# Optimization experiments

Measured on AMD Instinct MI355X. Metric: run time of the kernel, lower is better.

Reference implementation:

```python
import jax, jax.numpy as jnp
import numpy as np

N_MOL, N_ATOM, DEG = 32, 128, 32
N = N_MOL * N_ATOM          # 4096 real atoms (no blanks)
P = N * DEG                 # 131072 pairs
N_SENS = 20
SOFT_MIN, SOFT_MAX, HARD_MAX = 0.7, 5.0, 7.5
N_IN, N_OUT, N_HIST = 2, 3, 3
NF1 = 20                    # hipnn1 n_features
NF0 = 2 * NF1               # hipnn0 n_features (doubled in __init__)
NG = 4 * NF1                # gate logits width of InteractLayer W
N_ATOM_LAYERS = 3
NIN0 = 2 + N_HIST           # one-hot over {1,8} + x_h channels


def setup_inputs():
    rng = np.random.default_rng(0)
    species = 1 + 7 * rng.integers(0, 2, size=(N_MOL, N_ATOM))  # values in {1,8}, all nonblank
    base = np.repeat(np.arange(N), DEG)
    local = base % N_ATOM
    neigh = (local + 1 + rng.integers(0, N_ATOM - 1, size=P)) % N_ATOM  # neighbor != self
    pair_second = (base // N_ATOM) * N_ATOM + neigh                     # same-molecule pairs
    key = jax.random.key(0)
    ks = jax.random.split(key, 20)
    g = lambda i, shape, s=0.1: jax.random.normal(ks[i], shape, dtype=jnp.float32) * s
    return {
        "species": jnp.asarray(species, jnp.int32),
        "coordinates": jax.random.uniform(ks[0], (N_MOL, N_ATOM, 3), jnp.float32, 0.0, 6.0),
        "x_h": g(1, (N_MOL, N_ATOM, N_HIST)),
        "x_raw": g(2, (N_MOL, N_ATOM, N_IN)),
        "pair_first": jnp.asarray(base, jnp.int32),
        "pair_second": jnp.asarray(pair_second, jnp.int32),
        "h0_int_w": g(3, (N_SENS, NIN0, NF0)),
        "h0_self_w": g(4, (NIN0, NF0)),
        "h0_self_b": g(5, (NF0,)),
        "h0_aw": g(6, (N_ATOM_LAYERS, NF0, NF0)),
        "h0_ab": g(7, (N_ATOM_LAYERS, NF0)),
        "h1_int_w": g(8, (N_SENS, 1, NF1)),
        "h1_self_w": g(9, (1, NF1)),
        "h1_self_b": g(10, (NF1,)),
        "h1_aw": g(11, (N_ATOM_LAYERS, NF1, NF1)),
        "h1_ab": g(12, (N_ATOM_LAYERS, NF1)),
        "W_int_w": g(13, (N_SENS, NF0, NG)),
        "W_self_w": g(14, (NF0, NG)),
        "W_self_b": g(15, (NG,)),
        "pw0": g(16, (NIN0, 1)),
        "pw1": g(17, (NF1, 1)),
        "pb1": g(18, (1,)),
    }


def _sensitivity(d):
    # inverse-distance gaussian sensitivities with smooth hard cutoff
    mu = jnp.linspace(1.0 / SOFT_MAX, 1.0 / SOFT_MIN, N_SENS)
    sigma = (1.0 / SOFT_MIN - 1.0 / SOFT_MAX) / N_SENS
    sense = jnp.exp(-0.5 * jnp.square((1.0 / d[:, None] - mu) / sigma))
    cut = jnp.where(d < HARD_MAX, jnp.square(jnp.cos(jnp.pi * d / (2.0 * HARD_MAX))), 0.0)
    return sense * cut[:, None]                                     # (P, n_sens)


def _interact(x, sense, pf, ps, int_w, self_w, self_b):
    # gather neighbor features, weight by sensitivities, scatter-add to center atom
    msg = sense[:, :, None] * x[ps][:, None, :]                     # (P, ns, fin)
    env = jax.ops.segment_sum(msg, pf, num_segments=N)              # (N, ns, fin)
    ns, fin, fout = int_w.shape
    return env.reshape(N, ns * fin) @ int_w.reshape(ns * fin, fout) + x @ self_w + self_b


def _hipnn(x, sense, pf, ps, int_w, self_w, self_b, aw, ab):
    y = jax.nn.softplus(_interact(x, sense, pf, ps, int_w, self_w, self_b))
    for i in range(aw.shape[0]):
        y = jax.nn.softplus(y @ aw[i] + ab[i])
    return x, y   # (input features, final block features)


def _forward(coordinates, x_h, x_raw,
             h0_int_w, h0_self_w, h0_self_b, h0_aw, h0_ab,
             h1_int_w, h1_self_w, h1_self_b, h1_aw, h1_ab,
             W_int_w, W_self_w, W_self_b, pw0, pw1, pb1,
             species, pair_first, pair_second):
    enc = (species.reshape(-1)[:, None] == jnp.array([1, 8])).astype(jnp.float32)  # OneHotSpecies
    coord = coordinates.reshape(-1, 3)
    diff = coord[pair_first] - coord[pair_second]
    d = jnp.sqrt(jnp.sum(diff * diff, axis=-1) + 1e-12)
    sense = _sensitivity(d)
    ind_f = jnp.concatenate([enc, x_h.reshape(N, N_HIST)], axis=1)  # (N, 5)
    f0_in, f0_out = _hipnn(ind_f, sense, pair_first, pair_second,
                           h0_int_w, h0_self_w, h0_self_b, h0_aw, h0_ab)
    c_t, h_t = f0_out[:, : NF0 // 2], f0_out[:, NF0 // 2:]

    def onestep(x_in, h_t, c_t):
        x_t = _hipnn(x_in, sense, pair_first, pair_second,
                     h1_int_w, h1_self_w, h1_self_b, h1_aw, h1_ab)[1]
        tmp = _interact(jnp.concatenate([x_t, h_t], axis=-1), sense,
                        pair_first, pair_second, W_int_w, W_self_w, W_self_b)
        tmp = tmp.reshape(N, NF1, 4)
        o_t = jax.nn.sigmoid(tmp[..., 3])
        c_t = jax.nn.sigmoid(tmp[..., 1]) * c_t + jax.nn.sigmoid(tmp[..., 0]) * jnp.tanh(tmp[..., 2])
        h_t = o_t * jnp.tanh(c_t)
        return o_t, h_t, c_t

    xr = x_raw.reshape(N, N_IN)
    o_t = None
    for t in range(N_IN):
        o_t, h_t, c_t = onestep(xr[:, t:t + 1], h_t, c_t)
    x0 = f0_in @ pw0 + o_t @ pw1 + pb1                              # PredictAtom
    outs = []
    for t in range(N_OUT):
        o_t, h_t, c_t = onestep(x0, h_t, c_t)
        x0 = f0_in @ pw0 + o_t @ pw1 + pb1
        outs.append(x0)
    return jnp.concatenate(outs, axis=-1)                           # (N, n_out)


def reference(species, coordinates, x_h, x_raw, pair_first, pair_second,
              h0_int_w, h0_self_w, h0_self_b, h0_aw, h0_ab,
              h1_int_w, h1_self_w, h1_self_b, h1_aw, h1_ab,
              W_int_w, W_self_w, W_self_b, pw0, pw1, pb1):
    return _forward(coordinates, x_h, x_raw,
                    h0_int_w, h0_self_w, h0_self_b, h0_aw, h0_ab,
                    h1_int_w, h1_self_w, h1_self_b, h1_aw, h1_ab,
                    W_int_w, W_self_w, W_self_b, pw0, pw1, pb1,
                    species, pair_first, pair_second)
```

## Files before the change

### kernel.cpp

```cpp
#include <hip/hip_runtime.h>
#include <hip/hip_bf16.h>


#define DEG 32
#define NA 4096
#define NP 131072

typedef __hip_bfloat16 bf16;
typedef __attribute__((ext_vector_type(8))) short short8v;
typedef __attribute__((ext_vector_type(4))) float f32x4;

#define Z0F 16.27906976744186f
#define DZ  1.0526315789473684f

__device__ __forceinline__ float frcp(float x){ return __builtin_amdgcn_rcpf(x); }
__device__ __forceinline__ float sigmoid_f(float x){ return frcp(1.f + __expf(-x)); }
__device__ __forceinline__ float tanh_f(float x){ return 1.f - 2.f*frcp(__expf(2.f*x)+1.f); }
__device__ __forceinline__ float softplus_f(float x){ return fmaxf(x,0.f) + __logf(1.f + __expf(-fabsf(x))); }
__device__ __forceinline__ unsigned bf16pack(float lo, float hi){
  unsigned ul = __float_as_uint(lo), uh = __float_as_uint(hi);
  unsigned rl = (ul + 0x7fffu + ((ul>>16)&1u)) >> 16;
  unsigned rh = (uh + 0x7fffu + ((uh>>16)&1u)) & 0xffff0000u;
  return rl | rh;
}
__device__ __forceinline__ unsigned short b16u(float v){
  unsigned u = __float_as_uint(v);
  return (unsigned short)((u + 0x7fffu + ((u>>16)&1u)) >> 16);
}

__global__ __launch_bounds__(256) void k_prep(
    const int* __restrict__ pf, const int* __restrict__ ps,
    const int* __restrict__ species,
    const float* __restrict__ coord, const float* __restrict__ xh,
    const float* __restrict__ pw0, const float* __restrict__ pb1,
    const float* __restrict__ Wint, const float* __restrict__ Wself,
    unsigned short* __restrict__ svA, unsigned* __restrict__ svB,
    bf16* __restrict__ Wmf, float* __restrict__ indf, float* __restrict__ proj0)
{
  int b = blockIdx.x, t = threadIdx.x;
  if (b < 512){
    int p = b*256 + t;
    int i = pf[p], j = ps[p];
    float dx = coord[i*3+0]-coord[j*3+0];
    float dy = coord[i*3+1]-coord[j*3+1];
    float dz = coord[i*3+2]-coord[j*3+2];
    float d = sqrtf(dx*dx+dy*dy+dz*dz + 1e-12f);
    float cu = 0.f;
    if (d < 7.5f){ float c = __cosf(d * 0.20943951023931953f); cu = c*c; }
    float z0 = (1.f/d - 0.2f)*Z0F;
    int atom = p>>5, k = p&31;
    float sv[20];
    #pragma unroll
    for(int s=0;s<20;s++){
      float z = z0 - (float)s*DZ;
      sv[s] = cu*__expf(-0.5f*z*z);
    }
    #pragma unroll
    for(int s=0;s<20;s++) svA[atom*640 + s*32 + k] = b16u(sv[s]);
    #pragma unroll
    for(int s2=0;s2<10;s2++) svB[atom*320 + k*10 + s2] = bf16pack(sv[2*s2], sv[2*s2+1]);
  } else if (b < 782){
    int tid = (b-512)*256 + t;
    if (tid < 69120){
      int j = tid & 7, l = (tid>>3) & 63, gt = (tid>>9)%5, slab = tid/2560;
      int k = slab*32 + ((l>>4)<<3) + j;
      int g = gt*16 + (l&15);
      float v = 0.f;
      if (k < 800)      v = Wint[k*80+g];
      else if (k < 840) v = Wself[(k-800)*80+g];
      Wmf[tid] = __float2bfloat16(v);
    }
  } else {
    int tid = (b-782)*256 + t;
    if (tid < NA){
      int sp = species[tid];
      float f0 = (sp==1)?1.f:0.f, f1 = (sp==8)?1.f:0.f;
      float f2=xh[tid*3+0], f3=xh[tid*3+1], f4=xh[tid*3+2];
      indf[tid*5+0]=f0; indf[tid*5+1]=f1; indf[tid*5+2]=f2;
      indf[tid*5+3]=f3; indf[tid*5+4]=f4;
      proj0[tid] = pb1[0] + f0*pw0[0] + f1*pw0[1] + f2*pw0[2]
                 + f3*pw0[3] + f4*pw0[4];
    }
  }
}

#define F_SVT  0
#define F_INDF 10432
#define F_ENV0 11072
#define F_Y0A  12672
#define F_Y0B  13312
#define F_NB   13952
#define F_SMEM 14080
__global__ __launch_bounds__(512) void k_f0(
    const int* __restrict__ ps, const unsigned* __restrict__ svB,
    const float* __restrict__ indf_g,
    const float* __restrict__ h0_iw, const float* __restrict__ h0_sw,
    const float* __restrict__ h0_sb, const float* __restrict__ h0_aw,
    const float* __restrict__ h0_ab,
    float* __restrict__ c_g, unsigned* __restrict__ h_p)
{
  __shared__ float smem[F_SMEM];
  const int t = threadIdx.x;
  const int mol = blockIdx.x & 31, sib = blockIdx.x >> 5;
  const int nbase = mol*128;
  const int abase = nbase + sib*16;
  float* svt  = smem + F_SVT;
  float* indf = smem + F_INDF;
  float* env0 = smem + F_ENV0;
  float* y0a  = smem + F_Y0A;
  float* y0b  = smem + F_Y0B;
  unsigned char* nb8 = (unsigned char*)(smem + F_NB);

  for(int i=t;i<5120;i+=512){
    int a=i/320, q=i%320, k=q/10, s2=q%10;
    unsigned v = svB[(abase+a)*320 + q];
    float* dst = svt + a*652 + k*20 + s2*2;
    dst[0] = __uint_as_float(v<<16);
    dst[1] = __uint_as_float(v & 0xffff0000u);
  }
  for(int i=t;i<640;i+=512) indf[i] = indf_g[nbase*5 + i];
  if (t < 512) nb8[t] = (unsigned char)(ps[abase*DEG + t] - nbase);
  __syncthreads();

  for(int task=t; task<1600; task+=512){
    int a = task/100, e = task%100, s = e/5, f = e%5;
    const float* svr = svt + a*652;
    const unsigned char* nbr = nb8 + a*32;
    float acc = 0.f;
    for(int k=0;k<32;k++) acc += svr[k*20+s]*indf[nbr[k]*5+f];
    env0[a*100+e] = acc;
  }
  __syncthreads();
  for(int task=t; task<640; task+=512){
    int a=task/40, o=task%40, row=(sib*16)+a;
    float acc = h0_sb[o];
    #pragma unroll
    for(int f=0;f<5;f++) acc += indf[row*5+f]*h0_sw[f*40+o];
    for(int e=0;e<100;e++) acc += env0[a*100+e]*h0_iw[e*40+o];
    y0a[a*40+o] = softplus_f(acc);
  }
  __syncthreads();
  float* cur = y0a; float* nxt = y0b;
  for(int l=0;l<3;l++){
    for(int task=t; task<640; task+=512){
      int a=task/40, o=task%40;
      float acc = h0_ab[l*40+o];
      for(int f=0;f<40;f++) acc += cur[a*40+f]*h0_aw[l*1600+f*40+o];
      nxt[a*40+o] = softplus_f(acc);
    }
    __syncthreads();
    float* tswap=cur; cur=nxt; nxt=tswap;
  }
  if (t < 320){ int a=t/20,u=t%20; c_g[(abase+a)*20+u] = cur[a*40+u]; }
  if (t < 160){ int a=t/10,p=t%10;
    h_p[NA*10 + (abase+a)*10+p] = bf16pack(cur[a*40+20+2*p], cur[a*40+21+2*p]); }
}

#define X_XIN 0
#define X_NB  128
#define X_WTS 256
#define X_EV1 1956
#define X_YA  2276
#define X_YB  2596
#define X_SMEM 2916
__global__ __launch_bounds__(320) void k_xt(
    const int* __restrict__ ps, const unsigned short* __restrict__ svA,
    const float* __restrict__ xraw, const float* __restrict__ x0g,
    int use_raw, int col,
    const float* __restrict__ h1_iw, const float* __restrict__ h1_sw,
    const float* __restrict__ h1_sb, const float* __restrict__ h1_aw,
    const float* __restrict__ h1_ab,
    unsigned* __restrict__ xt_p)
{
  __shared__ float smem[X_SMEM];
  const int t = threadIdx.x;
  const int mol = blockIdx.x & 31, sib = blockIdx.x >> 5;
  const int nbase = mol*128;
  const int abase = nbase + sib*16;
  float* xin = smem + X_XIN;
  unsigned char* nb8 = (unsigned char*)(smem + X_NB);
  float* wts = smem + X_WTS;
  float* ev1 = smem + X_EV1;
  float* yA  = smem + X_YA;
  float* yB  = smem + X_YB;

  if (t < 128) xin[t] = use_raw ? xraw[(nbase+t)*2+col] : x0g[nbase+t];
  for(int i=t;i<512;i+=320) nb8[i] = (unsigned char)(ps[abase*DEG+i] - nbase);
  for(int i=t;i<1700;i+=320){
    float v;
    if(i<400){ int o=i/20,s=i%20; v=h1_iw[s*20+o]; }
    else if(i<420) v=h1_sw[i-400];
    else if(i<440) v=h1_sb[i-420];
    else if(i<1640){ int q=i-440,L=q/400,rem=q%400,o=rem/20,f=rem%20; v=h1_aw[L*400+f*20+o]; }
    else v=h1_ab[i-1640];
    wts[i]=v;
  }
  __syncthreads();

  {
    int a=t/20, s=t%20;
    const uint4* sp4 = (const uint4*)(svA + (abase+a)*640 + s*32);
    const unsigned char* nbr = nb8 + a*32;
    float acc = 0.f;
    #pragma unroll
    for(int c4=0;c4<4;c4++){
      uint4 w = sp4[c4];
      unsigned wu[4] = {w.x,w.y,w.z,w.w};
      #pragma unroll
      for(int j=0;j<4;j++){
        float flo = __uint_as_float(wu[j]<<16);
        float fhi = __uint_as_float(wu[j] & 0xffff0000u);
        int k = c4*8 + 2*j;
        acc += flo*xin[nbr[k]] + fhi*xin[nbr[k+1]];
      }
    }
    ev1[t] = acc;
  }
  __syncthreads();
  {
    int a=t/20, o=t%20;
    float acc = wts[420+o] + xin[sib*16+a]*wts[400+o];
    const float* e = ev1 + a*20; const float* w = wts + o*20;
    #pragma unroll
    for(int s=0;s<20;s++) acc += e[s]*w[s];
    yA[t] = softplus_f(acc);
  }
  __syncthreads();
  #pragma unroll
  for(int L=0;L<2;L++){
    const float* src = (L==0)? yA : yB;
    float* dst       = (L==0)? yB : yA;
    int a=t/20, o=t%20;
    float acc = wts[1640+L*20+o];
    const float* sr = src + a*20; const float* w = wts + 440 + L*400 + o*20;
    #pragma unroll
    for(int f=0;f<20;f++) acc += sr[f]*w[f];
    dst[t] = softplus_f(acc);
    __syncthreads();
  }
  if (t < 160){
    int a=t/10, p=t%10, o0=2*p, o1=o0+1;
    const float* e = yA + a*20;
    float a0 = wts[1680+o0], a1 = wts[1680+o1];
    const float* wA = wts + 1240 + o0*20;
    const float* wB = wA + 20;
    #pragma unroll
    for(int f=0;f<20;f++){ a0 += e[f]*wA[f]; a1 += e[f]*wB[f]; }
    xt_p[(abase+a)*10+p] = bf16pack(softplus_f(a0), softplus_f(a1));
  }
}

#define E_XHP 0
#define E_NB  2560
#define E_PRJ 2688
#define E_PW1 2704
#define E_AR  2728
#define E_ER  E_AR
#define E_TMP (E_AR+6976)
#define E_RED (E_TMP+1280)
#define E_HT  (E_RED+320)
#define E_SMEM (E_AR+10432)
__global__ __launch_bounds__(512) void k_env(
    const int* __restrict__ ps, const unsigned* __restrict__ svB,
    const unsigned* __restrict__ xt_p, const unsigned* __restrict__ h_p,
    int rpar, int wpar,
    const bf16* __restrict__ Wmf, const float* __restrict__ Wb,
    const float* __restrict__ pw1, const float* __restrict__ proj0,
    float* __restrict__ c_g, unsigned* __restrict__ h_po,
    float* __restrict__ x0g, float* __restrict__ outp, int out_col)
{
  __shared__ float smem[E_SMEM];
  const int t = threadIdx.x;
  const int mol = blockIdx.x & 31, sib = blockIdx.x >> 5;
  const int nbase = mol*128;
  const int abase = nbase + sib*16;
  unsigned* xhp = (unsigned*)(smem + E_XHP);
  unsigned char* nb8 = (unsigned char*)(smem + E_NB);
  float* prj  = smem + E_PRJ;
  float* pw1s = smem + E_PW1;
  float* svt  = smem + E_AR;

  for(int i=t;i<1280;i+=512){
    int r=i/10, p=i%10;
    xhp[r*20+p]    = xt_p[(nbase+r)*10+p];
    xhp[r*20+10+p] = h_p[rpar*NA*10 + (nbase+r)*10+p];
  }
  if (t < 512) nb8[t] = (unsigned char)(ps[abase*DEG + t] - nbase);
  for(int i=t;i<5120;i+=512){
    int a=i/320, q=i%320, k=q/10, s2=q%10;
    unsigned v = svB[(abase+a)*320 + q];
    float* dst = svt + a*652 + k*20 + s2*2;
    dst[0] = __uint_as_float(v<<16);
    dst[1] = __uint_as_float(v & 0xffff0000u);
  }
  if (t < 16) prj[t] = proj0[abase+t];
  if (t < 20) pw1s[t] = pw1[t];
  __syncthreads();

  float accE[20][2]; unsigned selfp = 0;
  if (t < 320){
    int a=t/20, f2=t%20;
    #pragma unroll
    for(int s=0;s<20;s++){ accE[s][0]=0.f; accE[s][1]=0.f; }
    const float* svr = svt + a*652;
    const unsigned char* nbr = nb8 + a*32;
    for(int k=0;k<32;k++){
      unsigned xp = xhp[nbr[k]*20 + f2];
      float xlo = __uint_as_float(xp<<16);
      float xhi = __uint_as_float(xp & 0xffff0000u);
      const float4* sq = (const float4*)(svr + k*20);
      float4 q0=sq[0],q1=sq[1],q2=sq[2],q3=sq[3],q4=sq[4];
      float sv[20]={q0.x,q0.y,q0.z,q0.w, q1.x,q1.y,q1.z,q1.w,
                    q2.x,q2.y,q2.z,q2.w, q3.x,q3.y,q3.z,q3.w,
                    q4.x,q4.y,q4.z,q4.w};
      #pragma unroll
      for(int s=0;s<20;s++){ accE[s][0] += sv[s]*xlo; accE[s][1] += sv[s]*xhi; }
    }
    selfp = xhp[(sib*16+a)*20 + f2];
  }
  __syncthreads();
  unsigned* er = (unsigned*)(smem + E_ER);
  if (t < 320){
    int a=t/20, f2=t%20;
    unsigned* e = er + a*436;
    #pragma unroll
    for(int s=0;s<20;s++) e[s*20+f2] = bf16pack(accE[s][0], accE[s][1]);
    e[400+f2] = selfp;
  }
  if (t < 256) er[(t>>4)*436 + 420 + (t&15)] = 0u;
  __syncthreads();

  float* tmp_s = smem + E_TMP;
  if (t < 320){
    int wv = t >> 6, l = t & 63;
    f32x4 cacc = {0.f,0.f,0.f,0.f};
    const unsigned* abase_p = er + (l & 15)*436 + ((l>>4)<<2);
    const short8v* bptr = (const short8v*)Wmf + (wv*64 + l);
    #pragma unroll 3
    for(int slab=0; slab<27; ++slab){
      short8v av = *(const short8v*)(abase_p + slab*16);
      short8v bv = bptr[slab*320];
      cacc = __builtin_amdgcn_mfma_f32_16x16x32_bf16(av, bv, cacc, 0,0,0);
    }
    int g = wv*16 + (l & 15);
    float wb = Wb[g];
    int r0 = (l>>4)*4;
    #pragma unroll
    for(int r=0;r<4;r++) tmp_s[(r0+r)*80 + g] = cacc[r] + wb;
  }
  __syncthreads();

  float* red = smem + E_RED;
  float* ht  = smem + E_HT;
  if (t < 320){
    int a=t/20, u=t%20;
    float4 tv = *(const float4*)(tmp_s + a*80 + u*4);
    float cold = c_g[(abase+a)*20+u];
    float cnew = sigmoid_f(tv.y)*cold + sigmoid_f(tv.x)*tanh_f(tv.z);
    float og   = sigmoid_f(tv.w);
    c_g[(abase+a)*20+u] = cnew;
    ht[a*20+u]  = og*tanh_f(cnew);
    red[a*20+u] = og*pw1s[u];
  }
  __syncthreads();
  if (t < 160){
    int a=t/10, p=t%10;
    h_po[wpar*NA*10 + (abase+a)*10+p] = bf16pack(ht[a*20+2*p], ht[a*20+2*p+1]);
  }
  if (t < 16){
    float accx = prj[t];
    #pragma unroll
    for(int u=0;u<20;u++) accx += red[t*20+u];
    x0g[abase+t] = accx;
    if (out_col >= 0) outp[(abase+t)*3+out_col] = accx;
  }
}

extern "C" void kernel_launch(void* const* d_in, const int* in_sizes, int n_in,
                              void* d_out, int out_size, void* d_ws, size_t ws_size,
                              hipStream_t stream)
{
  const int*   species = (const int*)  d_in[0];
  const float* coord   = (const float*)d_in[1];
  const float* xh      = (const float*)d_in[2];
  const float* xraw    = (const float*)d_in[3];
  const int*   pf      = (const int*)  d_in[4];
  const int*   ps      = (const int*)  d_in[5];
  const float* h0_intw = (const float*)d_in[6];
  const float* h0_sw   = (const float*)d_in[7];
  const float* h0_sb   = (const float*)d_in[8];
  const float* h0_aw   = (const float*)d_in[9];
  const float* h0_ab   = (const float*)d_in[10];
  const float* h1_intw = (const float*)d_in[11];
  const float* h1_sw   = (const float*)d_in[12];
  const float* h1_sb   = (const float*)d_in[13];
  const float* h1_aw   = (const float*)d_in[14];
  const float* h1_ab   = (const float*)d_in[15];
  const float* W_intw  = (const float*)d_in[16];
  const float* W_sw    = (const float*)d_in[17];
  const float* W_sb    = (const float*)d_in[18];
  const float* pw0     = (const float*)d_in[19];
  const float* pw1     = (const float*)d_in[20];
  const float* pb1     = (const float*)d_in[21];
  float* outp = (float*)d_out;

  float* w = (float*)d_ws;
  unsigned short* svA = (unsigned short*)w;  w += NA*320;
  unsigned* svB = (unsigned*)w;              w += NA*320;
  bf16* Wmf = (bf16*)w;                      w += 34560;
  float* indf = w;                           w += NA*5;
  float* proj0 = w;                          w += NA;
  unsigned* xt_p = (unsigned*)w;             w += NA*10;
  unsigned* h_p = (unsigned*)w;              w += 2*NA*10;
  float* x0g = w;                            w += NA;
  float* c_g = w;                            w += NA*20;

  k_prep<<<800,256,0,stream>>>(pf,ps,species,coord,xh,pw0,pb1,W_intw,W_sw,
                               svA,svB,Wmf,indf,proj0);
  k_f0<<<256,512,0,stream>>>(ps,svB,indf,h0_intw,h0_sw,h0_sb,h0_aw,h0_ab,
                             c_g,h_p);
  for(int step=0; step<5; ++step){
    int use_raw = (step<2)?1:0, col = (step<2)? step : 0;
    int rpar = (step+1)&1, wpar = step&1;
    int out_col = (step>=2)? (step-2) : -1;
    k_xt<<<256,320,0,stream>>>(ps,svA,xraw,x0g,use_raw,col,
                               h1_intw,h1_sw,h1_sb,h1_aw,h1_ab, xt_p);
    k_env<<<256,512,0,stream>>>(ps,svB,xt_p,h_p,rpar,wpar,
                                Wmf,W_sb,pw1,proj0,
                                c_g,h_p,x0g,outp,out_col);
  }
}
```

Measured before the change: 112.5 us.

## Use MFMA for neighbor-sensitivity aggregation and fuse input-driven xt steps into f0 launch

The per-atom envelope contraction over 32 neighbors in k_env moves from scalar FMAs over an LDS-unpacked sensitivity tile to bf16 MFMA 16x16x32 ops. The A operand is a new pre-swizzled Amf layout that k_prep writes once. Separately, the two x_raw-driven xt computations, which do not depend on the recurrence, now run in the same launch as the f0 setup, with double-buffered xt outputs, removing two kernel launches and serial dependencies. The cost is extra workspace for Amf, more shuffles and stores in k_prep, and a larger block for k_xt.

```diff
diff --git a/kernel.cpp b/kernel.cpp
--- a/kernel.cpp
+++ b/kernel.cpp
@@ -27,6 +27,19 @@
   unsigned u = __float_as_uint(v);
   return (unsigned short)((u + 0x7fffu + ((u>>16)&1u)) >> 16);
 }
+union UU { unsigned u[4]; short8v v; };
+union U4 { uint4 q; short8v v; unsigned u[4]; };
+
+__device__ __forceinline__ void wr_tile(unsigned* er, f32x4 D, int M, int N,
+                                        int lg, int lr, int l){
+  #pragma unroll
+  for(int r=0;r<4;r++){
+    float vd = D[r];
+    float pr = __shfl_xor(vd, 1);
+    int s = M*16 + lg*4 + r, f = N*16 + lr;
+    if(!(l&1) && s<20 && f<40) er[s*20 + (f>>1)] = bf16pack(vd, pr);
+  }
+}
 
 __global__ __launch_bounds__(256) void k_prep(
     const int* __restrict__ pf, const int* __restrict__ ps,
@@ -35,6 +48,7 @@
     const float* __restrict__ pw0, const float* __restrict__ pb1,
     const float* __restrict__ Wint, const float* __restrict__ Wself,
     unsigned short* __restrict__ svA, unsigned* __restrict__ svB,
+    unsigned* __restrict__ Amf,
     bf16* __restrict__ Wmf, float* __restrict__ indf, float* __restrict__ proj0)
 {
   int b = blockIdx.x, t = threadIdx.x;
@@ -49,16 +63,34 @@
     if (d < 7.5f){ float c = __cosf(d * 0.20943951023931953f); cu = c*c; }
     float z0 = (1.f/d - 0.2f)*Z0F;
     int atom = p>>5, k = p&31;
-    float sv[20];
+    float sv[20], svn[20];
     #pragma unroll
     for(int s=0;s<20;s++){
       float z = z0 - (float)s*DZ;
       sv[s] = cu*__expf(-0.5f*z*z);
     }
     #pragma unroll
+    for(int s=0;s<20;s++) svn[s] = __shfl_down(sv[s], 1);
+    #pragma unroll
     for(int s=0;s<20;s++) svA[atom*640 + s*32 + k] = b16u(sv[s]);
     #pragma unroll
     for(int s2=0;s2<10;s2++) svB[atom*320 + k*10 + s2] = bf16pack(sv[2*s2], sv[2*s2+1]);
+    if (!(k&1)){
+      int lg = k>>3, q = (k>>1)&3;
+      #pragma unroll
+      for(int s=0;s<20;s++){
+        int lr = s&15, fr = s>>4;
+        Amf[atom*512 + (lg*16+lr)*8 + fr*4 + q] = bf16pack(sv[s], svn[s]);
+      }
+    } else {
+      int idx = k>>1;
+      int lg2 = idx>>2, q2 = idx&3;
+      #pragma unroll
+      for(int j2=0;j2<12;j2++){
+        int lr = 4+j2;
+        Amf[atom*512 + (lg2*16+lr)*8 + 4 + q2] = 0u;
+      }
+    }
   } else if (b < 782){
     int tid = (b-512)*256 + t;
     if (tid < 69120){
@@ -91,7 +123,7 @@
 #define F_Y0B  13312
 #define F_NB   13952
 #define F_SMEM 14080
-__global__ __launch_bounds__(512) void k_f0(
+__device__ void f0_body(float* smem, int t, int mol, int sib,
     const int* __restrict__ ps, const unsigned* __restrict__ svB,
     const float* __restrict__ indf_g,
     const float* __restrict__ h0_iw, const float* __restrict__ h0_sw,
@@ -99,9 +131,6 @@
     const float* __restrict__ h0_ab,
     float* __restrict__ c_g, unsigned* __restrict__ h_p)
 {
-  __shared__ float smem[F_SMEM];
-  const int t = threadIdx.x;
-  const int mol = blockIdx.x & 31, sib = blockIdx.x >> 5;
   const int nbase = mol*128;
   const int abase = nbase + sib*16;
   float* svt  = smem + F_SVT;
@@ -162,8 +191,7 @@
 #define X_EV1 1956
 #define X_YA  2276
 #define X_YB  2596
-#define X_SMEM 2916
-__global__ __launch_bounds__(320) void k_xt(
+__device__ void xt_body(float* smem, int t, int mol, int sib,
     const int* __restrict__ ps, const unsigned short* __restrict__ svA,
     const float* __restrict__ xraw, const float* __restrict__ x0g,
     int use_raw, int col,
@@ -172,9 +200,6 @@
     const float* __restrict__ h1_ab,
     unsigned* __restrict__ xt_p)
 {
-  __shared__ float smem[X_SMEM];
-  const int t = threadIdx.x;
-  const int mol = blockIdx.x & 31, sib = blockIdx.x >> 5;
   const int nbase = mol*128;
   const int abase = nbase + sib*16;
   float* xin = smem + X_XIN;
@@ -185,8 +210,8 @@
   float* yB  = smem + X_YB;
 
   if (t < 128) xin[t] = use_raw ? xraw[(nbase+t)*2+col] : x0g[nbase+t];
-  for(int i=t;i<512;i+=320) nb8[i] = (unsigned char)(ps[abase*DEG+i] - nbase);
-  for(int i=t;i<1700;i+=320){
+  if (t < 512) nb8[t] = (unsigned char)(ps[abase*DEG+t] - nbase);
+  for(int i=t;i<1700;i+=512){
     float v;
     if(i<400){ int o=i/20,s=i%20; v=h1_iw[s*20+o]; }
     else if(i<420) v=h1_sw[i-400];
@@ -197,7 +222,7 @@
   }
   __syncthreads();
 
-  {
+  if (t < 320){
     int a=t/20, s=t%20;
     const uint4* sp4 = (const uint4*)(svA + (abase+a)*640 + s*32);
     const unsigned char* nbr = nb8 + a*32;
@@ -217,7 +242,7 @@
     ev1[t] = acc;
   }
   __syncthreads();
-  {
+  if (t < 320){
     int a=t/20, o=t%20;
     float acc = wts[420+o] + xin[sib*16+a]*wts[400+o];
     const float* e = ev1 + a*20; const float* w = wts + o*20;
@@ -230,12 +255,14 @@
   for(int L=0;L<2;L++){
     const float* src = (L==0)? yA : yB;
     float* dst       = (L==0)? yB : yA;
-    int a=t/20, o=t%20;
-    float acc = wts[1640+L*20+o];
-    const float* sr = src + a*20; const float* w = wts + 440 + L*400 + o*20;
-    #pragma unroll
-    for(int f=0;f<20;f++) acc += sr[f]*w[f];
-    dst[t] = softplus_f(acc);
+    if (t < 320){
+      int a=t/20, o=t%20;
+      float acc = wts[1640+L*20+o];
+      const float* sr = src + a*20; const float* w = wts + 440 + L*400 + o*20;
+      #pragma unroll
+      for(int f=0;f<20;f++) acc += sr[f]*w[f];
+      dst[t] = softplus_f(acc);
+    }
     __syncthreads();
   }
   if (t < 160){
@@ -250,18 +277,58 @@
   }
 }
 
+__global__ __launch_bounds__(512) void k_fx(
+    const int* __restrict__ ps, const unsigned* __restrict__ svB,
+    const unsigned short* __restrict__ svA,
+    const float* __restrict__ indf_g, const float* __restrict__ xraw,
+    const float* __restrict__ h0_iw, const float* __restrict__ h0_sw,
+    const float* __restrict__ h0_sb, const float* __restrict__ h0_aw,
+    const float* __restrict__ h0_ab,
+    const float* __restrict__ h1_iw, const float* __restrict__ h1_sw,
+    const float* __restrict__ h1_sb, const float* __restrict__ h1_aw,
+    const float* __restrict__ h1_ab,
+    float* __restrict__ c_g, unsigned* __restrict__ h_p,
+    unsigned* __restrict__ xt_p0, unsigned* __restrict__ xt_p1)
+{
+  __shared__ float smem[F_SMEM];
+  const int t = threadIdx.x;
+  const int sel = blockIdx.x >> 8;
+  const int blk = blockIdx.x & 255;
+  const int mol = blk & 31, sib = blk >> 5;
+  if (sel == 0)
+    f0_body(smem, t, mol, sib, ps, svB, indf_g,
+            h0_iw,h0_sw,h0_sb,h0_aw,h0_ab, c_g, h_p);
+  else
+    xt_body(smem, t, mol, sib, ps, svA, xraw, (const float*)0, 1, sel-1,
+            h1_iw,h1_sw,h1_sb,h1_aw,h1_ab, (sel==1)? xt_p0 : xt_p1);
+}
+
+__global__ __launch_bounds__(512) void k_xt(
+    const int* __restrict__ ps, const unsigned short* __restrict__ svA,
+    const float* __restrict__ xraw, const float* __restrict__ x0g,
+    const float* __restrict__ h1_iw, const float* __restrict__ h1_sw,
+    const float* __restrict__ h1_sb, const float* __restrict__ h1_aw,
+    const float* __restrict__ h1_ab,
+    unsigned* __restrict__ xt_p)
+{
+  __shared__ float smem[2916];
+  const int t = threadIdx.x;
+  const int mol = blockIdx.x & 31, sib = blockIdx.x >> 5;
+  xt_body(smem, t, mol, sib, ps, svA, xraw, x0g, 0, 0,
+          h1_iw,h1_sw,h1_sb,h1_aw,h1_ab, xt_p);
+}
+
 #define E_XHP 0
 #define E_NB  2560
 #define E_PRJ 2688
 #define E_PW1 2704
-#define E_AR  2728
-#define E_ER  E_AR
-#define E_TMP (E_AR+6976)
-#define E_RED (E_TMP+1280)
-#define E_HT  (E_RED+320)
-#define E_SMEM (E_AR+10432)
+#define E_ER  2728
+#define E_TMP 9704
+#define E_RED 10984
+#define E_HT  11304
+#define E_SMEM 11624
 __global__ __launch_bounds__(512) void k_env(
-    const int* __restrict__ ps, const unsigned* __restrict__ svB,
+    const int* __restrict__ ps, const unsigned* __restrict__ Amf,
     const unsigned* __restrict__ xt_p, const unsigned* __restrict__ h_p,
     int rpar, int wpar,
     const bf16* __restrict__ Wmf, const float* __restrict__ Wb,
@@ -278,7 +345,7 @@
   unsigned char* nb8 = (unsigned char*)(smem + E_NB);
   float* prj  = smem + E_PRJ;
   float* pw1s = smem + E_PW1;
-  float* svt  = smem + E_AR;
+  unsigned* er = (unsigned*)(smem + E_ER);
 
   for(int i=t;i<1280;i+=512){
     int r=i/10, p=i%10;
@@ -286,47 +353,67 @@
     xhp[r*20+10+p] = h_p[rpar*NA*10 + (nbase+r)*10+p];
   }
   if (t < 512) nb8[t] = (unsigned char)(ps[abase*DEG + t] - nbase);
-  for(int i=t;i<5120;i+=512){
-    int a=i/320, q=i%320, k=q/10, s2=q%10;
-    unsigned v = svB[(abase+a)*320 + q];
-    float* dst = svt + a*652 + k*20 + s2*2;
-    dst[0] = __uint_as_float(v<<16);
-    dst[1] = __uint_as_float(v & 0xffff0000u);
-  }
   if (t < 16) prj[t] = proj0[abase+t];
   if (t < 20) pw1s[t] = pw1[t];
   __syncthreads();
 
-  float accE[20][2]; unsigned selfp = 0;
-  if (t < 320){
-    int a=t/20, f2=t%20;
-    #pragma unroll
-    for(int s=0;s<20;s++){ accE[s][0]=0.f; accE[s][1]=0.f; }
-    const float* svr = svt + a*652;
-    const unsigned char* nbr = nb8 + a*32;
-    for(int k=0;k<32;k++){
-      unsigned xp = xhp[nbr[k]*20 + f2];
-      float xlo = __uint_as_float(xp<<16);
-      float xhi = __uint_as_float(xp & 0xffff0000u);
-      const float4* sq = (const float4*)(svr + k*20);
-      float4 q0=sq[0],q1=sq[1],q2=sq[2],q3=sq[3],q4=sq[4];
-      float sv[20]={q0.x,q0.y,q0.z,q0.w, q1.x,q1.y,q1.z,q1.w,
-                    q2.x,q2.y,q2.z,q2.w, q3.x,q3.y,q3.z,q3.w,
-                    q4.x,q4.y,q4.z,q4.w};
+  {
+    const int wv = t>>6, l = t&63, lg = (t>>4)&3, lr = t&15;
+    f32x4 z4 = {0.f,0.f,0.f,0.f};
+    #pragma unroll
+    for(int ai=0; ai<2; ++ai){
+      int a = wv*2 + ai;
+      int atom_g = abase + a;
+      const U4* ap = (const U4*)(Amf + (unsigned)atom_g*512u + (unsigned)l*8u);
+      U4 A0 = ap[0], A1 = ap[1];
+      const unsigned* nbw = (const unsigned*)(nb8 + a*32 + lg*8);
+      unsigned nw0=nbw[0], nw1=nbw[1];
+      int nl[8];
       #pragma unroll
-      for(int s=0;s<20;s++){ accE[s][0] += sv[s]*xlo; accE[s][1] += sv[s]*xhi; }
-    }
-    selfp = xhp[(sib*16+a)*20 + f2];
-  }
-  __syncthreads();
-  unsigned* er = (unsigned*)(smem + E_ER);
-  if (t < 320){
-    int a=t/20, f2=t%20;
-    unsigned* e = er + a*436;
-    #pragma unroll
-    for(int s=0;s<20;s++) e[s*20+f2] = bf16pack(accE[s][0], accE[s][1]);
-    e[400+f2] = selfp;
-  }
+      for(int j2=0;j2<4;j2++){ nl[j2]=(nw0>>(8*j2))&255; nl[4+j2]=(nw1>>(8*j2))&255; }
+      f32x4 d00,d01,d02,d10,d11,d12;
+      {
+        UU B; int f=lr; unsigned sh=(f&1)<<4;
+        #pragma unroll
+        for(int q=0;q<4;q++){
+          unsigned wlo = xhp[nl[2*q]*20 + (f>>1)];
+          unsigned whi = xhp[nl[2*q+1]*20 + (f>>1)];
+          B.u[q] = ((wlo>>sh)&0xffffu) | (((whi>>sh)&0xffffu)<<16);
+        }
+        d00=__builtin_amdgcn_mfma_f32_16x16x32_bf16(A0.v,B.v,z4,0,0,0);
+        d10=__builtin_amdgcn_mfma_f32_16x16x32_bf16(A1.v,B.v,z4,0,0,0);
+      }
+      {
+        UU B; int f=16+lr; unsigned sh=(f&1)<<4;
+        #pragma unroll
+        for(int q=0;q<4;q++){
+          unsigned wlo = xhp[nl[2*q]*20 + (f>>1)];
+          unsigned whi = xhp[nl[2*q+1]*20 + (f>>1)];
+          B.u[q] = ((wlo>>sh)&0xffffu) | (((whi>>sh)&0xffffu)<<16);
+        }
+        d01=__builtin_amdgcn_mfma_f32_16x16x32_bf16(A0.v,B.v,z4,0,0,0);
+        d11=__builtin_amdgcn_mfma_f32_16x16x32_bf16(A1.v,B.v,z4,0,0,0);
+      }
+      {
+        UU B; int f=32+lr; unsigned sh=(f&1)<<4; int val=(f<40);
+        #pragma unroll
+        for(int q=0;q<4;q++){
+          if (val){
+            unsigned wlo = xhp[nl[2*q]*20 + (f>>1)];
+            unsigned whi = xhp[nl[2*q+1]*20 + (f>>1)];
+            B.u[q] = ((wlo>>sh)&0xffffu) | (((whi>>sh)&0xffffu)<<16);
+          } else B.u[q] = 0u;
+        }
+        d02=__builtin_amdgcn_mfma_f32_16x16x32_bf16(A0.v,B.v,z4,0,0,0);
+        d12=__builtin_amdgcn_mfma_f32_16x16x32_bf16(A1.v,B.v,z4,0,0,0);
+      }
+      unsigned* era = er + a*436;
+      wr_tile(era,d00,0,0,lg,lr,l); wr_tile(era,d01,0,1,lg,lr,l);
+      wr_tile(era,d02,0,2,lg,lr,l); wr_tile(era,d10,1,0,lg,lr,l);
+      wr_tile(era,d11,1,1,lg,lr,l); wr_tile(era,d12,1,2,lg,lr,l);
+    }
+  }
+  if (t < 320){ int a=t/20, f2=t%20; er[a*436+400+f2] = xhp[(sib*16+a)*20+f2]; }
   if (t < 256) er[(t>>4)*436 + 420 + (t&15)] = 0u;
   __syncthreads();
 
@@ -407,25 +494,30 @@
   float* w = (float*)d_ws;
   unsigned short* svA = (unsigned short*)w;  w += NA*320;
   unsigned* svB = (unsigned*)w;              w += NA*320;
+  unsigned* Amf = (unsigned*)w;              w += NA*512;
   bf16* Wmf = (bf16*)w;                      w += 34560;
   float* indf = w;                           w += NA*5;
   float* proj0 = w;                          w += NA;
-  unsigned* xt_p = (unsigned*)w;             w += NA*10;
+  unsigned* xt_pA = (unsigned*)w;            w += NA*10;
+  unsigned* xt_pB = (unsigned*)w;            w += NA*10;
   unsigned* h_p = (unsigned*)w;              w += 2*NA*10;
   float* x0g = w;                            w += NA;
   float* c_g = w;                            w += NA*20;
 
   k_prep<<<800,256,0,stream>>>(pf,ps,species,coord,xh,pw0,pb1,W_intw,W_sw,
-                               svA,svB,Wmf,indf,proj0);
-  k_f0<<<256,512,0,stream>>>(ps,svB,indf,h0_intw,h0_sw,h0_sb,h0_aw,h0_ab,
-                             c_g,h_p);
+                               svA,svB,Amf,Wmf,indf,proj0);
+  k_fx<<<768,512,0,stream>>>(ps,svB,svA,indf,xraw,
+                             h0_intw,h0_sw,h0_sb,h0_aw,h0_ab,
+                             h1_intw,h1_sw,h1_sb,h1_aw,h1_ab,
+                             c_g,h_p,xt_pA,xt_pB);
   for(int step=0; step<5; ++step){
-    int use_raw = (step<2)?1:0, col = (step<2)? step : 0;
     int rpar = (step+1)&1, wpar = step&1;
     int out_col = (step>=2)? (step-2) : -1;
-    k_xt<<<256,320,0,stream>>>(ps,svA,xraw,x0g,use_raw,col,
-                               h1_intw,h1_sw,h1_sb,h1_aw,h1_ab, xt_p);
-    k_env<<<256,512,0,stream>>>(ps,svB,xt_p,h_p,rpar,wpar,
+    unsigned* xtp = (step&1)? xt_pB : xt_pA;
+    if (step >= 2)
+      k_xt<<<256,512,0,stream>>>(ps,svA,xraw,x0g,
+                                 h1_intw,h1_sw,h1_sb,h1_aw,h1_ab, xtp);
+    k_env<<<256,512,0,stream>>>(ps,Amf,xtp,h_p,rpar,wpar,
                                 Wmf,W_sb,pw1,proj0,
                                 c_g,h_p,x0g,outp,out_col);
   }
```

Result: faster. 105.9 us (-5.8%).
